# Kernel tuning notes

Hardware: AMD Instinct MI355X
Metric: run time of the kernel (lower is better)

Reference implementation:

```python
import jax, jax.numpy as jnp
import numpy as np

B, L, S, H, E = 4, 2048, 2048, 8, 64


def setup_inputs() -> dict:
    key = jax.random.key(0)
    kq, kk, kv, kt = jax.random.split(key, 4)
    queries = jax.random.normal(kq, (B, L, H, E), dtype=jnp.float32)
    keys = jax.random.normal(kk, (B, S, H, E), dtype=jnp.float32)
    values = jax.random.normal(kv, (B, S, H, E), dtype=jnp.float32)
    # de-stationarization log-scale factor, kept small so exp(tau) ~ O(1)
    tau = 0.1 * jax.random.normal(kt, (B, 1, 1, 1), dtype=jnp.float32)
    # causal mask: True above the diagonal (positions to be masked)
    attn_mask = jnp.triu(jnp.ones((L, S), dtype=bool), k=1)
    return {"queries": queries, "keys": keys, "values": values,
            "attn_mask": attn_mask, "tau": tau}


def reference(queries, keys, values, attn_mask, tau):
    # queries: [B,L,H,E], keys/values: [B,S,H,E], tau: [B,1,1,1], mask: [L,S]
    E_ = queries.shape[-1]
    scale = 1.0 / jnp.sqrt(jnp.asarray(E_, dtype=queries.dtype))
    # scores: [B,H,L,S], with tau-based de-stationarization rescale
    scores = jnp.einsum('blhe,bshe->bhls', queries, keys) * (scale * jnp.exp(tau))
    scores = jnp.where(attn_mask, -jnp.inf, scores)
    A = jax.nn.softmax(scores, axis=-1)  # dropout is identity at inference
    V = jnp.einsum('bhls,bshd->blhd', A, values)
    return V
```

## Files before the change

### kernel.cpp

```cpp
#include <hip/hip_runtime.h>
#include <hip/hip_bf16.h>
#include <math.h>

#define B_ 4
#define L_ 2048
#define H_ 8
#define E_ 64
#define HE 512

typedef short bf16x8 __attribute__((ext_vector_type(8)));
typedef float f32x4 __attribute__((ext_vector_type(4)));
typedef float f32x16 __attribute__((ext_vector_type(16)));
typedef unsigned short u16x4 __attribute__((ext_vector_type(4)));
typedef unsigned short u16x8 __attribute__((ext_vector_type(8)));

__device__ __forceinline__ unsigned short f2b(float f) {
  return __builtin_bit_cast(unsigned short, (__hip_bfloat16)f);
}
__device__ __forceinline__ unsigned cvtpk(float lo, float hi) {
  unsigned r;
  asm("v_cvt_pk_bf16_f32 %0, %1, %2" : "=v"(r) : "v"(lo), "v"(hi));
  return r;
}
__device__ __forceinline__ void pl32swap(unsigned &a, unsigned &b) {
  asm volatile("v_permlane32_swap_b32 %0, %1" : "+v"(a), "+v"(b));
}

__global__ __launch_bounds__(256, 2) void attn_fwd(
    const float* __restrict__ Q, const float* __restrict__ K,
    const float* __restrict__ V, const float* __restrict__ tau,
    float* __restrict__ O)
{
  const int f  = blockIdx.x + 16 * (blockIdx.y + 8 * blockIdx.z);
  const int u  = f >> 5, hb = f & 31;
  const int h  = hb & 7, b = hb >> 3;
  const int qt = (u < 8) ? u : 23 - u;

  const int tid  = threadIdx.x;
  const int wave = tid >> 6, lane = tid & 63;
  const int l31 = lane & 31, hi = lane >> 5;
  const int l7 = l31 & 7;

  __shared__ unsigned short ldsK[2][64 * 64];
  __shared__ unsigned short ldsV[2][64 * 64];

  const float qscale = 0.125f * expf(tau[b]) * 1.44269504088896f;
  const int q0w = qt * 128 + wave * 32;
  const int myq = q0w + l31;

  const float* Qb = Q + (((size_t)b * L_ + myq) * H_ + h) * E_;
  bf16x8 qf[4];
  #pragma unroll
  for (int ks = 0; ks < 4; ++ks) {
    f32x4 a = *(const f32x4*)(Qb + ks * 16 + hi * 8);
    f32x4 c = *(const f32x4*)(Qb + ks * 16 + hi * 8 + 4);
    #pragma unroll
    for (int j = 0; j < 4; ++j) {
      qf[ks][j]     = (short)f2b(a[j] * qscale);
      qf[ks][4 + j] = (short)f2b(c[j] * qscale);
    }
  }

  float m_run = -INFINITY, l_run = 0.0f;
  f32x16 oacc[2];
  #pragma unroll
  for (int nd = 0; nd < 2; ++nd)
    #pragma unroll
    for (int r = 0; r < 16; ++r) oacc[nd][r] = 0.0f;

  const int krow = tid >> 2, kcg = tid & 3;
  const int vkv = (tid & 15) * 4, vd = (tid >> 4) * 4;
  const float* Kp = K + ((size_t)b * L_ * H_ + h) * E_ + (size_t)krow * HE + kcg * 16;
  const float* Vp = V + ((size_t)b * L_ * H_ + h) * E_ + (size_t)vkv * HE + vd;
  const int kwo0 = krow * 64 + (((2 * kcg) ^ (krow & 7)) << 3);
  const int kwo1 = krow * 64 + (((2 * kcg + 1) ^ (krow & 7)) << 3);

  const int nt = 2 * qt + 2;
  const int tmaxw = 2 * qt + (wave >> 1);

  {
    f32x4 kq[4], vq[4];
    #pragma unroll
    for (int i = 0; i < 4; ++i) kq[i] = *(const f32x4*)(Kp + 4 * i);
    #pragma unroll
    for (int i = 0; i < 4; ++i) vq[i] = *(const f32x4*)(Vp + (size_t)i * HE);
    u16x8 w0, w1;
    #pragma unroll
    for (int j = 0; j < 4; ++j) {
      w0[j] = f2b(kq[0][j]); w0[4 + j] = f2b(kq[1][j]);
      w1[j] = f2b(kq[2][j]); w1[4 + j] = f2b(kq[3][j]);
    }
    *(u16x8*)(&ldsK[0][kwo0]) = w0;
    *(u16x8*)(&ldsK[0][kwo1]) = w1;
    #pragma unroll
    for (int jd = 0; jd < 4; ++jd) {
      const int row = vd + jd;
      u16x4 vw;
      #pragma unroll
      for (int i = 0; i < 4; ++i) vw[i] = f2b(vq[i][jd]);
      *(u16x4*)(&ldsV[0][row * 64 + (((vkv >> 3) ^ (row & 7)) << 3) + (vkv & 7)]) = vw;
    }
  }
  __syncthreads();
  int cur = 0;

  for (int t = 0; t < nt; ++t) {
    const bool havenext = (t + 1 < nt);
    f32x4 kq[4], vq[4];
    if (havenext) {
      const float* Kn = Kp + (size_t)(t + 1) * 64 * HE;
      const float* Vn = Vp + (size_t)(t + 1) * 64 * HE;
      #pragma unroll
      for (int i = 0; i < 4; ++i) kq[i] = *(const f32x4*)(Kn + 4 * i);
      #pragma unroll
      for (int i = 0; i < 4; ++i) vq[i] = *(const f32x4*)(Vn + (size_t)i * HE);
    }

    if (t <= tmaxw) {
      const unsigned short* Kl = ldsK[cur];
      const unsigned short* Vl = ldsV[cur];

      f32x16 sacc[2];
      #pragma unroll
      for (int mt = 0; mt < 2; ++mt)
        #pragma unroll
        for (int r = 0; r < 16; ++r) sacc[mt][r] = 0.0f;
      __builtin_amdgcn_s_setprio(1);
      #pragma unroll
      for (int ks = 0; ks < 4; ++ks) {
        #pragma unroll
        for (int mt = 0; mt < 2; ++mt) {
          bf16x8 kf = *(const bf16x8*)(Kl + (32 * mt + l31) * 64 +
                                       (((2 * ks + hi) ^ l7) << 3));
          sacc[mt] = __builtin_amdgcn_mfma_f32_32x32x16_bf16(kf, qf[ks], sacc[mt], 0, 0, 0);
        }
      }
      __builtin_amdgcn_s_setprio(0);

      if (t == tmaxw) {
        const int dq = myq - 64 * t;
        const int kvhi = 4 * hi;
        #pragma unroll
        for (int mt = 0; mt < 2; ++mt)
          #pragma unroll
          for (int r = 0; r < 16; ++r) {
            const int kvl = (r & 3) + 8 * (r >> 2) + 32 * mt;
            if (kvl + kvhi > dq) sacc[mt][r] = -3.0e38f;
          }
      }

      float p0 = sacc[0][0], p1 = sacc[0][1], p2 = sacc[0][2], p3 = sacc[0][3];
      #pragma unroll
      for (int mt = 0; mt < 2; ++mt)
        #pragma unroll
        for (int r = (mt == 0 ? 4 : 0); r < 16; r += 4) {
          p0 = fmaxf(p0, sacc[mt][r]);
          p1 = fmaxf(p1, sacc[mt][r + 1]);
          p2 = fmaxf(p2, sacc[mt][r + 2]);
          p3 = fmaxf(p3, sacc[mt][r + 3]);
        }
      float mx = fmaxf(fmaxf(p0, p1), fmaxf(p2, p3));
      mx = fmaxf(mx, __shfl_xor(mx, 32));

      if (!__all(mx - m_run <= 8.0f)) {
        const float mnew = fmaxf(m_run, mx);
        const float corr = exp2f(m_run - mnew);
        m_run = mnew;
        l_run *= corr;
        #pragma unroll
        for (int r = 0; r < 16; ++r) {
          const int qrow = (r & 3) + 8 * (r >> 2) + 4 * hi;
          const float cr = __shfl(corr, qrow);
          oacc[0][r] *= cr;
          oacc[1][r] *= cr;
        }
      }

      float s0 = 0.f, s1 = 0.f, s2 = 0.f, s3 = 0.f;
      #pragma unroll
      for (int mt = 0; mt < 2; ++mt)
        #pragma unroll
        for (int r = 0; r < 16; r += 4) {
          float e0 = exp2f(sacc[mt][r]     - m_run);
          float e1 = exp2f(sacc[mt][r + 1] - m_run);
          float e2 = exp2f(sacc[mt][r + 2] - m_run);
          float e3 = exp2f(sacc[mt][r + 3] - m_run);
          sacc[mt][r] = e0; sacc[mt][r + 1] = e1;
          sacc[mt][r + 2] = e2; sacc[mt][r + 3] = e3;
          s0 += e0; s1 += e1; s2 += e2; s3 += e3;
        }
      float rs = (s0 + s1) + (s2 + s3);
      rs += __shfl_xor(rs, 32);
      l_run += rs;

      unsigned pk0[8], pk1[8];
      #pragma unroll
      for (int i = 0; i < 8; ++i) pk0[i] = cvtpk(sacc[0][2 * i], sacc[0][2 * i + 1]);
      #pragma unroll
      for (int i = 0; i < 8; ++i) pk1[i] = cvtpk(sacc[1][2 * i], sacc[1][2 * i + 1]);
      bf16x8 pf[4];
      #pragma unroll
      for (int ks = 0; ks < 4; ++ks) {
        unsigned a  = (ks >> 1) ? pk1[4 * (ks & 1)]     : pk0[4 * (ks & 1)];
        unsigned y  = (ks >> 1) ? pk1[4 * (ks & 1) + 2] : pk0[4 * (ks & 1) + 2];
        unsigned a2 = (ks >> 1) ? pk1[4 * (ks & 1) + 1] : pk0[4 * (ks & 1) + 1];
        unsigned y2 = (ks >> 1) ? pk1[4 * (ks & 1) + 3] : pk0[4 * (ks & 1) + 3];
        pl32swap(a, y);
        pl32swap(a2, y2);
        union { unsigned w[4]; bf16x8 v; } pu;
        pu.w[0] = a; pu.w[1] = a2; pu.w[2] = y; pu.w[3] = y2;
        pf[ks] = pu.v;
      }

      __builtin_amdgcn_s_setprio(1);
      #pragma unroll
      for (int ks = 0; ks < 4; ++ks) {
        #pragma unroll
        for (int nd = 0; nd < 2; ++nd) {
          bf16x8 vf = *(const bf16x8*)(Vl + (32 * nd + l31) * 64 +
                                       (((2 * ks + hi) ^ l7) << 3));
          oacc[nd] = __builtin_amdgcn_mfma_f32_32x32x16_bf16(pf[ks], vf, oacc[nd], 0, 0, 0);
        }
      }
      __builtin_amdgcn_s_setprio(0);
    }

    if (havenext) {
      const int nb = cur ^ 1;
      u16x8 w0, w1;
      #pragma unroll
      for (int j = 0; j < 4; ++j) {
        w0[j] = f2b(kq[0][j]); w0[4 + j] = f2b(kq[1][j]);
        w1[j] = f2b(kq[2][j]); w1[4 + j] = f2b(kq[3][j]);
      }
      *(u16x8*)(&ldsK[nb][kwo0]) = w0;
      *(u16x8*)(&ldsK[nb][kwo1]) = w1;
      #pragma unroll
      for (int jd = 0; jd < 4; ++jd) {
        const int row = vd + jd;
        u16x4 vw;
        #pragma unroll
        for (int i = 0; i < 4; ++i) vw[i] = f2b(vq[i][jd]);
        *(u16x4*)(&ldsV[nb][row * 64 + (((vkv >> 3) ^ (row & 7)) << 3) + (vkv & 7)]) = vw;
      }
      __syncthreads();
      cur = nb;
    }
  }

  const float linv = 1.0f / l_run;
  float* Ob = O + (((size_t)b * L_ + q0w) * H_ + h) * E_;
  #pragma unroll
  for (int r = 0; r < 16; ++r) {
    const int qrow = (r & 3) + 8 * (r >> 2) + 4 * hi;
    const float inv = __shfl(linv, qrow);
    Ob[(size_t)qrow * HE + l31]      = oacc[0][r] * inv;
    Ob[(size_t)qrow * HE + 32 + l31] = oacc[1][r] * inv;
  }
}

extern "C" void kernel_launch(void* const* d_in, const int* in_sizes, int n_in,
                              void* d_out, int out_size, void* d_ws, size_t ws_size,
                              hipStream_t stream) {
  (void)in_sizes; (void)n_in; (void)out_size; (void)d_ws; (void)ws_size;
  const float* Q   = (const float*)d_in[0];
  const float* K   = (const float*)d_in[1];
  const float* V   = (const float*)d_in[2];
  const float* tau = (const float*)d_in[4];
  float* O = (float*)d_out;
  dim3 grid(L_ / 128, H_, B_), block(256);
  hipLaunchKernelGGL(attn_fwd, grid, block, 0, stream, Q, K, V, tau, O);
}
```

Measured before the change: 60.08 us.

## Widen KV tile to 128 keys per iteration with 16-way V swizzle

Each loop iteration now stages 128 keys and values into LDS instead of 64, which halves the number of iterations and barriers. The QK product now covers four 32-row tiles, and the PV product is reorganised over eight k-steps with a 128-wide transposed V layout and a 16-row XOR swizzle. Per-wave causal skipping is removed, so every wave computes the full final tile and relies on masking. This roughly doubles LDS use and register pressure (more score accumulators and prefetch registers), which may hurt occupancy at two blocks per CU.

```diff
diff --git a/kernel.cpp b/kernel.cpp
--- a/kernel.cpp
+++ b/kernel.cpp
@@ -41,12 +41,13 @@
   const int l31 = lane & 31, hi = lane >> 5;
   const int l7 = l31 & 7;
 
-  __shared__ unsigned short ldsK[2][64 * 64];
-  __shared__ unsigned short ldsV[2][64 * 64];
+  __shared__ unsigned short ldsK[2][128 * 64];
+  __shared__ unsigned short ldsV[2][64 * 128];
 
   const float qscale = 0.125f * expf(tau[b]) * 1.44269504088896f;
   const int q0w = qt * 128 + wave * 32;
   const int myq = q0w + l31;
+  const int dqd = 32 * wave + l31;
 
   const float* Qb = Q + (((size_t)b * L_ + myq) * H_ + h) * E_;
   bf16x8 qf[4];
@@ -72,33 +73,35 @@
   const int vkv = (tid & 15) * 4, vd = (tid >> 4) * 4;
   const float* Kp = K + ((size_t)b * L_ * H_ + h) * E_ + (size_t)krow * HE + kcg * 16;
   const float* Vp = V + ((size_t)b * L_ * H_ + h) * E_ + (size_t)vkv * HE + vd;
-  const int kwo0 = krow * 64 + (((2 * kcg) ^ (krow & 7)) << 3);
-  const int kwo1 = krow * 64 + (((2 * kcg + 1) ^ (krow & 7)) << 3);
-
-  const int nt = 2 * qt + 2;
-  const int tmaxw = 2 * qt + (wave >> 1);
-
-  {
-    f32x4 kq[4], vq[4];
-    #pragma unroll
-    for (int i = 0; i < 4; ++i) kq[i] = *(const f32x4*)(Kp + 4 * i);
-    #pragma unroll
-    for (int i = 0; i < 4; ++i) vq[i] = *(const f32x4*)(Vp + (size_t)i * HE);
+
+  const int nt = qt + 1;
+
+  f32x4 kq[2][4], vq[2][4];
+  #pragma unroll
+  for (int hf = 0; hf < 2; ++hf) {
+    #pragma unroll
+    for (int i = 0; i < 4; ++i) kq[hf][i] = *(const f32x4*)(Kp + hf * 64 * HE + 4 * i);
+    #pragma unroll
+    for (int i = 0; i < 4; ++i) vq[hf][i] = *(const f32x4*)(Vp + hf * 64 * HE + (size_t)i * HE);
+  }
+  #pragma unroll
+  for (int hf = 0; hf < 2; ++hf) {
+    const int r = krow + 64 * hf;
     u16x8 w0, w1;
     #pragma unroll
     for (int j = 0; j < 4; ++j) {
-      w0[j] = f2b(kq[0][j]); w0[4 + j] = f2b(kq[1][j]);
-      w1[j] = f2b(kq[2][j]); w1[4 + j] = f2b(kq[3][j]);
-    }
-    *(u16x8*)(&ldsK[0][kwo0]) = w0;
-    *(u16x8*)(&ldsK[0][kwo1]) = w1;
+      w0[j] = f2b(kq[hf][0][j]); w0[4 + j] = f2b(kq[hf][1][j]);
+      w1[j] = f2b(kq[hf][2][j]); w1[4 + j] = f2b(kq[hf][3][j]);
+    }
+    *(u16x8*)(&ldsK[0][r * 64 + (((2 * kcg) ^ (krow & 7)) << 3)]) = w0;
+    *(u16x8*)(&ldsK[0][r * 64 + (((2 * kcg + 1) ^ (krow & 7)) << 3)]) = w1;
     #pragma unroll
     for (int jd = 0; jd < 4; ++jd) {
       const int row = vd + jd;
       u16x4 vw;
       #pragma unroll
-      for (int i = 0; i < 4; ++i) vw[i] = f2b(vq[i][jd]);
-      *(u16x4*)(&ldsV[0][row * 64 + (((vkv >> 3) ^ (row & 7)) << 3) + (vkv & 7)]) = vw;
+      for (int i = 0; i < 4; ++i) vw[i] = f2b(vq[hf][i][jd]);
+      *(u16x4*)(&ldsV[0][row * 128 + ((((vkv >> 3) + 8 * hf) ^ (row & 15)) << 3) + (vkv & 7)]) = vw;
     }
   }
   __syncthreads();
@@ -106,142 +109,142 @@
 
   for (int t = 0; t < nt; ++t) {
     const bool havenext = (t + 1 < nt);
-    f32x4 kq[4], vq[4];
     if (havenext) {
-      const float* Kn = Kp + (size_t)(t + 1) * 64 * HE;
-      const float* Vn = Vp + (size_t)(t + 1) * 64 * HE;
-      #pragma unroll
-      for (int i = 0; i < 4; ++i) kq[i] = *(const f32x4*)(Kn + 4 * i);
-      #pragma unroll
-      for (int i = 0; i < 4; ++i) vq[i] = *(const f32x4*)(Vn + (size_t)i * HE);
-    }
-
-    if (t <= tmaxw) {
-      const unsigned short* Kl = ldsK[cur];
-      const unsigned short* Vl = ldsV[cur];
-
-      f32x16 sacc[2];
-      #pragma unroll
-      for (int mt = 0; mt < 2; ++mt)
-        #pragma unroll
-        for (int r = 0; r < 16; ++r) sacc[mt][r] = 0.0f;
-      __builtin_amdgcn_s_setprio(1);
-      #pragma unroll
-      for (int ks = 0; ks < 4; ++ks) {
-        #pragma unroll
-        for (int mt = 0; mt < 2; ++mt) {
-          bf16x8 kf = *(const bf16x8*)(Kl + (32 * mt + l31) * 64 +
-                                       (((2 * ks + hi) ^ l7) << 3));
-          sacc[mt] = __builtin_amdgcn_mfma_f32_32x32x16_bf16(kf, qf[ks], sacc[mt], 0, 0, 0);
+      const float* Kn = Kp + (size_t)(t + 1) * 128 * HE;
+      const float* Vn = Vp + (size_t)(t + 1) * 128 * HE;
+      #pragma unroll
+      for (int hf = 0; hf < 2; ++hf) {
+        #pragma unroll
+        for (int i = 0; i < 4; ++i) kq[hf][i] = *(const f32x4*)(Kn + hf * 64 * HE + 4 * i);
+        #pragma unroll
+        for (int i = 0; i < 4; ++i) vq[hf][i] = *(const f32x4*)(Vn + hf * 64 * HE + (size_t)i * HE);
+      }
+    }
+
+    const unsigned short* Kl = ldsK[cur];
+    const unsigned short* Vl = ldsV[cur];
+
+    f32x16 sacc[4];
+    #pragma unroll
+    for (int mt = 0; mt < 4; ++mt)
+      #pragma unroll
+      for (int r = 0; r < 16; ++r) sacc[mt][r] = 0.0f;
+    __builtin_amdgcn_s_setprio(1);
+    #pragma unroll
+    for (int ks = 0; ks < 4; ++ks) {
+      #pragma unroll
+      for (int mt = 0; mt < 4; ++mt) {
+        bf16x8 kf = *(const bf16x8*)(Kl + (32 * mt + l31) * 64 +
+                                     (((2 * ks + hi) ^ l7) << 3));
+        sacc[mt] = __builtin_amdgcn_mfma_f32_32x32x16_bf16(kf, qf[ks], sacc[mt], 0, 0, 0);
+      }
+    }
+    __builtin_amdgcn_s_setprio(0);
+
+    if (t == nt - 1) {
+      #pragma unroll
+      for (int mt = 0; mt < 4; ++mt)
+        #pragma unroll
+        for (int r = 0; r < 16; ++r) {
+          const int kvl = 32 * mt + (r & 3) + 8 * (r >> 2) + 4 * hi;
+          if (kvl > dqd) sacc[mt][r] = -3.0e38f;
         }
-      }
-      __builtin_amdgcn_s_setprio(0);
-
-      if (t == tmaxw) {
-        const int dq = myq - 64 * t;
-        const int kvhi = 4 * hi;
-        #pragma unroll
-        for (int mt = 0; mt < 2; ++mt)
-          #pragma unroll
-          for (int r = 0; r < 16; ++r) {
-            const int kvl = (r & 3) + 8 * (r >> 2) + 32 * mt;
-            if (kvl + kvhi > dq) sacc[mt][r] = -3.0e38f;
-          }
-      }
-
-      float p0 = sacc[0][0], p1 = sacc[0][1], p2 = sacc[0][2], p3 = sacc[0][3];
-      #pragma unroll
-      for (int mt = 0; mt < 2; ++mt)
-        #pragma unroll
-        for (int r = (mt == 0 ? 4 : 0); r < 16; r += 4) {
-          p0 = fmaxf(p0, sacc[mt][r]);
-          p1 = fmaxf(p1, sacc[mt][r + 1]);
-          p2 = fmaxf(p2, sacc[mt][r + 2]);
-          p3 = fmaxf(p3, sacc[mt][r + 3]);
-        }
-      float mx = fmaxf(fmaxf(p0, p1), fmaxf(p2, p3));
-      mx = fmaxf(mx, __shfl_xor(mx, 32));
-
-      if (!__all(mx - m_run <= 8.0f)) {
-        const float mnew = fmaxf(m_run, mx);
-        const float corr = exp2f(m_run - mnew);
-        m_run = mnew;
-        l_run *= corr;
-        #pragma unroll
-        for (int r = 0; r < 16; ++r) {
-          const int qrow = (r & 3) + 8 * (r >> 2) + 4 * hi;
-          const float cr = __shfl(corr, qrow);
-          oacc[0][r] *= cr;
-          oacc[1][r] *= cr;
-        }
-      }
-
-      float s0 = 0.f, s1 = 0.f, s2 = 0.f, s3 = 0.f;
-      #pragma unroll
-      for (int mt = 0; mt < 2; ++mt)
-        #pragma unroll
-        for (int r = 0; r < 16; r += 4) {
-          float e0 = exp2f(sacc[mt][r]     - m_run);
-          float e1 = exp2f(sacc[mt][r + 1] - m_run);
-          float e2 = exp2f(sacc[mt][r + 2] - m_run);
-          float e3 = exp2f(sacc[mt][r + 3] - m_run);
-          sacc[mt][r] = e0; sacc[mt][r + 1] = e1;
-          sacc[mt][r + 2] = e2; sacc[mt][r + 3] = e3;
-          s0 += e0; s1 += e1; s2 += e2; s3 += e3;
-        }
-      float rs = (s0 + s1) + (s2 + s3);
-      rs += __shfl_xor(rs, 32);
-      l_run += rs;
-
-      unsigned pk0[8], pk1[8];
-      #pragma unroll
-      for (int i = 0; i < 8; ++i) pk0[i] = cvtpk(sacc[0][2 * i], sacc[0][2 * i + 1]);
-      #pragma unroll
-      for (int i = 0; i < 8; ++i) pk1[i] = cvtpk(sacc[1][2 * i], sacc[1][2 * i + 1]);
-      bf16x8 pf[4];
-      #pragma unroll
-      for (int ks = 0; ks < 4; ++ks) {
-        unsigned a  = (ks >> 1) ? pk1[4 * (ks & 1)]     : pk0[4 * (ks & 1)];
-        unsigned y  = (ks >> 1) ? pk1[4 * (ks & 1) + 2] : pk0[4 * (ks & 1) + 2];
-        unsigned a2 = (ks >> 1) ? pk1[4 * (ks & 1) + 1] : pk0[4 * (ks & 1) + 1];
-        unsigned y2 = (ks >> 1) ? pk1[4 * (ks & 1) + 3] : pk0[4 * (ks & 1) + 3];
-        pl32swap(a, y);
-        pl32swap(a2, y2);
-        union { unsigned w[4]; bf16x8 v; } pu;
-        pu.w[0] = a; pu.w[1] = a2; pu.w[2] = y; pu.w[3] = y2;
-        pf[ks] = pu.v;
-      }
-
-      __builtin_amdgcn_s_setprio(1);
-      #pragma unroll
-      for (int ks = 0; ks < 4; ++ks) {
-        #pragma unroll
-        for (int nd = 0; nd < 2; ++nd) {
-          bf16x8 vf = *(const bf16x8*)(Vl + (32 * nd + l31) * 64 +
-                                       (((2 * ks + hi) ^ l7) << 3));
-          oacc[nd] = __builtin_amdgcn_mfma_f32_32x32x16_bf16(pf[ks], vf, oacc[nd], 0, 0, 0);
-        }
-      }
-      __builtin_amdgcn_s_setprio(0);
-    }
+    }
+
+    float p0 = sacc[0][0], p1 = sacc[0][1], p2 = sacc[0][2], p3 = sacc[0][3];
+    #pragma unroll
+    for (int mt = 0; mt < 4; ++mt)
+      #pragma unroll
+      for (int r = (mt == 0 ? 4 : 0); r < 16; r += 4) {
+        p0 = fmaxf(p0, sacc[mt][r]);
+        p1 = fmaxf(p1, sacc[mt][r + 1]);
+        p2 = fmaxf(p2, sacc[mt][r + 2]);
+        p3 = fmaxf(p3, sacc[mt][r + 3]);
+      }
+    float mx = fmaxf(fmaxf(p0, p1), fmaxf(p2, p3));
+    mx = fmaxf(mx, __shfl_xor(mx, 32));
+
+    if (!__all(mx - m_run <= 8.0f)) {
+      const float mnew = fmaxf(m_run, mx);
+      const float corr = exp2f(m_run - mnew);
+      m_run = mnew;
+      l_run *= corr;
+      #pragma unroll
+      for (int r = 0; r < 16; ++r) {
+        const int qrow = (r & 3) + 8 * (r >> 2) + 4 * hi;
+        const float cr = __shfl(corr, qrow);
+        oacc[0][r] *= cr;
+        oacc[1][r] *= cr;
+      }
+    }
+
+    float s0 = 0.f, s1 = 0.f, s2 = 0.f, s3 = 0.f;
+    #pragma unroll
+    for (int mt = 0; mt < 4; ++mt)
+      #pragma unroll
+      for (int r = 0; r < 16; r += 4) {
+        float e0 = exp2f(sacc[mt][r]     - m_run);
+        float e1 = exp2f(sacc[mt][r + 1] - m_run);
+        float e2 = exp2f(sacc[mt][r + 2] - m_run);
+        float e3 = exp2f(sacc[mt][r + 3] - m_run);
+        sacc[mt][r] = e0; sacc[mt][r + 1] = e1;
+        sacc[mt][r + 2] = e2; sacc[mt][r + 3] = e3;
+        s0 += e0; s1 += e1; s2 += e2; s3 += e3;
+      }
+    float rs = (s0 + s1) + (s2 + s3);
+    rs += __shfl_xor(rs, 32);
+    l_run += rs;
+
+    unsigned pk[4][8];
+    #pragma unroll
+    for (int mt = 0; mt < 4; ++mt)
+      #pragma unroll
+      for (int i = 0; i < 8; ++i)
+        pk[mt][i] = cvtpk(sacc[mt][2 * i], sacc[mt][2 * i + 1]);
+
+    __builtin_amdgcn_s_setprio(1);
+    #pragma unroll
+    for (int ks = 0; ks < 8; ++ks) {
+      const int c = ks & 1;
+      unsigned a  = pk[ks >> 1][4 * c];
+      unsigned y  = pk[ks >> 1][4 * c + 2];
+      unsigned a2 = pk[ks >> 1][4 * c + 1];
+      unsigned y2 = pk[ks >> 1][4 * c + 3];
+      pl32swap(a, y);
+      pl32swap(a2, y2);
+      union { unsigned w[4]; bf16x8 v; } pu;
+      pu.w[0] = a; pu.w[1] = a2; pu.w[2] = y; pu.w[3] = y2;
+      #pragma unroll
+      for (int nd = 0; nd < 2; ++nd) {
+        const int d = 32 * nd + l31;
+        bf16x8 vf = *(const bf16x8*)(Vl + d * 128 +
+                                     (((2 * ks + hi) ^ (d & 15)) << 3));
+        oacc[nd] = __builtin_amdgcn_mfma_f32_32x32x16_bf16(pu.v, vf, oacc[nd], 0, 0, 0);
+      }
+    }
+    __builtin_amdgcn_s_setprio(0);
 
     if (havenext) {
       const int nb = cur ^ 1;
-      u16x8 w0, w1;
-      #pragma unroll
-      for (int j = 0; j < 4; ++j) {
-        w0[j] = f2b(kq[0][j]); w0[4 + j] = f2b(kq[1][j]);
-        w1[j] = f2b(kq[2][j]); w1[4 + j] = f2b(kq[3][j]);
-      }
-      *(u16x8*)(&ldsK[nb][kwo0]) = w0;
-      *(u16x8*)(&ldsK[nb][kwo1]) = w1;
-      #pragma unroll
-      for (int jd = 0; jd < 4; ++jd) {
-        const int row = vd + jd;
-        u16x4 vw;
-        #pragma unroll
-        for (int i = 0; i < 4; ++i) vw[i] = f2b(vq[i][jd]);
-        *(u16x4*)(&ldsV[nb][row * 64 + (((vkv >> 3) ^ (row & 7)) << 3) + (vkv & 7)]) = vw;
+      #pragma unroll
+      for (int hf = 0; hf < 2; ++hf) {
+        const int r = krow + 64 * hf;
+        u16x8 w0, w1;
+        #pragma unroll
+        for (int j = 0; j < 4; ++j) {
+          w0[j] = f2b(kq[hf][0][j]); w0[4 + j] = f2b(kq[hf][1][j]);
+          w1[j] = f2b(kq[hf][2][j]); w1[4 + j] = f2b(kq[hf][3][j]);
+        }
+        *(u16x8*)(&ldsK[nb][r * 64 + (((2 * kcg) ^ (krow & 7)) << 3)]) = w0;
+        *(u16x8*)(&ldsK[nb][r * 64 + (((2 * kcg + 1) ^ (krow & 7)) << 3)]) = w1;
+        #pragma unroll
+        for (int jd = 0; jd < 4; ++jd) {
+          const int row = vd + jd;
+          u16x4 vw;
+          #pragma unroll
+          for (int i = 0; i < 4; ++i) vw[i] = f2b(vq[hf][i][jd]);
+          *(u16x4*)(&ldsV[nb][row * 128 + ((((vkv >> 3) + 8 * hf) ^ (row & 15)) << 3) + (vkv & 7)]) = vw;
+        }
       }
       __syncthreads();
       cur = nb;
```

Measured after the change: 63.86 us. +6.3%, slower.

## Split KV sequence across two wave groups per block and merge partial softmax

Applied to the files above, without the earlier changes.

Doubles the block to 512 threads so that two halves of 4 waves each process alternating 64-key tiles of the same 128-query tile. Each step now loads 128 keys, which halves the number of loop iterations and barriers per block. At the end the second half's partial outputs and row max/sum go to shared memory (a union with the KV buffers) and are merged flash-decoding style. The aim is more parallelism and latency hiding per query tile, at the cost of doubled LDS, an extra combine pass, and possible occupancy pressure from launch_bounds(512,4).

```diff
diff --git a/kernel.cpp b/kernel.cpp
--- a/kernel.cpp
+++ b/kernel.cpp
@@ -26,7 +26,7 @@
   asm volatile("v_permlane32_swap_b32 %0, %1" : "+v"(a), "+v"(b));
 }
 
-__global__ __launch_bounds__(256, 2) void attn_fwd(
+__global__ __launch_bounds__(512, 4) void attn_fwd(
     const float* __restrict__ Q, const float* __restrict__ K,
     const float* __restrict__ V, const float* __restrict__ tau,
     float* __restrict__ O)
@@ -40,13 +40,19 @@
   const int wave = tid >> 6, lane = tid & 63;
   const int l31 = lane & 31, hi = lane >> 5;
   const int l7 = l31 & 7;
-
-  __shared__ unsigned short ldsK[2][64 * 64];
-  __shared__ unsigned short ldsV[2][64 * 64];
+  const int half = wave >> 2, wv = wave & 3;
+
+  __shared__ union {
+    struct { unsigned short Kt[2][2][64 * 64];
+             unsigned short Vt[2][2][64 * 64]; } kv;
+    struct { float O[128][64]; float m[128]; float l[128]; } cmb;
+  } sm;
 
   const float qscale = 0.125f * expf(tau[b]) * 1.44269504088896f;
-  const int q0w = qt * 128 + wave * 32;
+  const int q0w = qt * 128 + wv * 32;
   const int myq = q0w + l31;
+  const int dqd = 32 * wv + l31 - 64 * half;
+  const bool skipw = (half == 1) && (wv < 2);
 
   const float* Qb = Q + (((size_t)b * L_ + myq) * H_ + h) * E_;
   bf16x8 qf[4];
@@ -68,37 +74,38 @@
     #pragma unroll
     for (int r = 0; r < 16; ++r) oacc[nd][r] = 0.0f;
 
-  const int krow = tid >> 2, kcg = tid & 3;
-  const int vkv = (tid & 15) * 4, vd = (tid >> 4) * 4;
-  const float* Kp = K + ((size_t)b * L_ * H_ + h) * E_ + (size_t)krow * HE + kcg * 16;
-  const float* Vp = V + ((size_t)b * L_ * H_ + h) * E_ + (size_t)vkv * HE + vd;
-  const int kwo0 = krow * 64 + (((2 * kcg) ^ (krow & 7)) << 3);
+  const int hs = tid >> 8, st = tid & 255;
+  const int krow = st >> 2, kcg = st & 3;
+  const int vkv = (st & 15) * 4, vd = (st >> 4) * 4;
+  const size_t bh = ((size_t)b * L_ * H_ + h) * E_;
+  const float* Kp = K + bh + (size_t)(64 * hs + krow) * HE + kcg * 16;
+  const float* Vp = V + bh + (size_t)(64 * hs + vkv) * HE + vd;
+  const int kwo0 = krow * 64 + (((2 * kcg)     ^ (krow & 7)) << 3);
   const int kwo1 = krow * 64 + (((2 * kcg + 1) ^ (krow & 7)) << 3);
 
-  const int nt = 2 * qt + 2;
-  const int tmaxw = 2 * qt + (wave >> 1);
-
+  const int nt = qt + 1;
+
+  f32x4 kq[4], vq[4];
+  #pragma unroll
+  for (int i = 0; i < 4; ++i) kq[i] = *(const f32x4*)(Kp + 4 * i);
+  #pragma unroll
+  for (int i = 0; i < 4; ++i) vq[i] = *(const f32x4*)(Vp + (size_t)i * HE);
   {
-    f32x4 kq[4], vq[4];
-    #pragma unroll
-    for (int i = 0; i < 4; ++i) kq[i] = *(const f32x4*)(Kp + 4 * i);
-    #pragma unroll
-    for (int i = 0; i < 4; ++i) vq[i] = *(const f32x4*)(Vp + (size_t)i * HE);
     u16x8 w0, w1;
     #pragma unroll
     for (int j = 0; j < 4; ++j) {
       w0[j] = f2b(kq[0][j]); w0[4 + j] = f2b(kq[1][j]);
       w1[j] = f2b(kq[2][j]); w1[4 + j] = f2b(kq[3][j]);
     }
-    *(u16x8*)(&ldsK[0][kwo0]) = w0;
-    *(u16x8*)(&ldsK[0][kwo1]) = w1;
+    *(u16x8*)(&sm.kv.Kt[hs][0][kwo0]) = w0;
+    *(u16x8*)(&sm.kv.Kt[hs][0][kwo1]) = w1;
     #pragma unroll
     for (int jd = 0; jd < 4; ++jd) {
       const int row = vd + jd;
       u16x4 vw;
       #pragma unroll
       for (int i = 0; i < 4; ++i) vw[i] = f2b(vq[i][jd]);
-      *(u16x4*)(&ldsV[0][row * 64 + (((vkv >> 3) ^ (row & 7)) << 3) + (vkv & 7)]) = vw;
+      *(u16x4*)(&sm.kv.Vt[hs][0][row * 64 + (((vkv >> 3) ^ (row & 7)) << 3) + (vkv & 7)]) = vw;
     }
   }
   __syncthreads();
@@ -106,19 +113,18 @@
 
   for (int t = 0; t < nt; ++t) {
     const bool havenext = (t + 1 < nt);
-    f32x4 kq[4], vq[4];
     if (havenext) {
-      const float* Kn = Kp + (size_t)(t + 1) * 64 * HE;
-      const float* Vn = Vp + (size_t)(t + 1) * 64 * HE;
+      const float* Kn = Kp + (size_t)(t + 1) * 128 * HE;
+      const float* Vn = Vp + (size_t)(t + 1) * 128 * HE;
       #pragma unroll
       for (int i = 0; i < 4; ++i) kq[i] = *(const f32x4*)(Kn + 4 * i);
       #pragma unroll
       for (int i = 0; i < 4; ++i) vq[i] = *(const f32x4*)(Vn + (size_t)i * HE);
     }
 
-    if (t <= tmaxw) {
-      const unsigned short* Kl = ldsK[cur];
-      const unsigned short* Vl = ldsV[cur];
+    if (!(skipw && t == nt - 1)) {
+      const unsigned short* Kl = sm.kv.Kt[half][cur];
+      const unsigned short* Vl = sm.kv.Vt[half][cur];
 
       f32x16 sacc[2];
       #pragma unroll
@@ -137,15 +143,13 @@
       }
       __builtin_amdgcn_s_setprio(0);
 
-      if (t == tmaxw) {
-        const int dq = myq - 64 * t;
-        const int kvhi = 4 * hi;
+      if (t == nt - 1) {
         #pragma unroll
         for (int mt = 0; mt < 2; ++mt)
           #pragma unroll
           for (int r = 0; r < 16; ++r) {
-            const int kvl = (r & 3) + 8 * (r >> 2) + 32 * mt;
-            if (kvl + kvhi > dq) sacc[mt][r] = -3.0e38f;
+            const int kvl = 32 * mt + (r & 3) + 8 * (r >> 2) + 4 * hi;
+            if (kvl > dqd) sacc[mt][r] = -3.0e38f;
           }
       }
 
@@ -193,33 +197,30 @@
       rs += __shfl_xor(rs, 32);
       l_run += rs;
 
-      unsigned pk0[8], pk1[8];
-      #pragma unroll
-      for (int i = 0; i < 8; ++i) pk0[i] = cvtpk(sacc[0][2 * i], sacc[0][2 * i + 1]);
-      #pragma unroll
-      for (int i = 0; i < 8; ++i) pk1[i] = cvtpk(sacc[1][2 * i], sacc[1][2 * i + 1]);
-      bf16x8 pf[4];
+      unsigned pk[2][8];
+      #pragma unroll
+      for (int mt = 0; mt < 2; ++mt)
+        #pragma unroll
+        for (int i = 0; i < 8; ++i)
+          pk[mt][i] = cvtpk(sacc[mt][2 * i], sacc[mt][2 * i + 1]);
+
+      __builtin_amdgcn_s_setprio(1);
       #pragma unroll
       for (int ks = 0; ks < 4; ++ks) {
-        unsigned a  = (ks >> 1) ? pk1[4 * (ks & 1)]     : pk0[4 * (ks & 1)];
-        unsigned y  = (ks >> 1) ? pk1[4 * (ks & 1) + 2] : pk0[4 * (ks & 1) + 2];
-        unsigned a2 = (ks >> 1) ? pk1[4 * (ks & 1) + 1] : pk0[4 * (ks & 1) + 1];
-        unsigned y2 = (ks >> 1) ? pk1[4 * (ks & 1) + 3] : pk0[4 * (ks & 1) + 3];
+        const int c = ks & 1, mtx = ks >> 1;
+        unsigned a  = pk[mtx][4 * c];
+        unsigned y  = pk[mtx][4 * c + 2];
+        unsigned a2 = pk[mtx][4 * c + 1];
+        unsigned y2 = pk[mtx][4 * c + 3];
         pl32swap(a, y);
         pl32swap(a2, y2);
         union { unsigned w[4]; bf16x8 v; } pu;
         pu.w[0] = a; pu.w[1] = a2; pu.w[2] = y; pu.w[3] = y2;
-        pf[ks] = pu.v;
-      }
-
-      __builtin_amdgcn_s_setprio(1);
-      #pragma unroll
-      for (int ks = 0; ks < 4; ++ks) {
         #pragma unroll
         for (int nd = 0; nd < 2; ++nd) {
           bf16x8 vf = *(const bf16x8*)(Vl + (32 * nd + l31) * 64 +
                                        (((2 * ks + hi) ^ l7) << 3));
-          oacc[nd] = __builtin_amdgcn_mfma_f32_32x32x16_bf16(pf[ks], vf, oacc[nd], 0, 0, 0);
+          oacc[nd] = __builtin_amdgcn_mfma_f32_32x32x16_bf16(pu.v, vf, oacc[nd], 0, 0, 0);
         }
       }
       __builtin_amdgcn_s_setprio(0);
@@ -233,29 +234,51 @@
         w0[j] = f2b(kq[0][j]); w0[4 + j] = f2b(kq[1][j]);
         w1[j] = f2b(kq[2][j]); w1[4 + j] = f2b(kq[3][j]);
       }
-      *(u16x8*)(&ldsK[nb][kwo0]) = w0;
-      *(u16x8*)(&ldsK[nb][kwo1]) = w1;
+      *(u16x8*)(&sm.kv.Kt[hs][nb][kwo0]) = w0;
+      *(u16x8*)(&sm.kv.Kt[hs][nb][kwo1]) = w1;
       #pragma unroll
       for (int jd = 0; jd < 4; ++jd) {
         const int row = vd + jd;
         u16x4 vw;
         #pragma unroll
         for (int i = 0; i < 4; ++i) vw[i] = f2b(vq[i][jd]);
-        *(u16x4*)(&ldsV[nb][row * 64 + (((vkv >> 3) ^ (row & 7)) << 3) + (vkv & 7)]) = vw;
+        *(u16x4*)(&sm.kv.Vt[hs][nb][row * 64 + (((vkv >> 3) ^ (row & 7)) << 3) + (vkv & 7)]) = vw;
       }
       __syncthreads();
       cur = nb;
     }
   }
 
-  const float linv = 1.0f / l_run;
-  float* Ob = O + (((size_t)b * L_ + q0w) * H_ + h) * E_;
-  #pragma unroll
-  for (int r = 0; r < 16; ++r) {
-    const int qrow = (r & 3) + 8 * (r >> 2) + 4 * hi;
-    const float inv = __shfl(linv, qrow);
-    Ob[(size_t)qrow * HE + l31]      = oacc[0][r] * inv;
-    Ob[(size_t)qrow * HE + 32 + l31] = oacc[1][r] * inv;
+  __syncthreads();
+  if (half == 1) {
+    #pragma unroll
+    for (int r = 0; r < 16; ++r) {
+      const int qrow = (r & 3) + 8 * (r >> 2) + 4 * hi;
+      sm.cmb.O[32 * wv + qrow][l31]      = oacc[0][r];
+      sm.cmb.O[32 * wv + qrow][32 + l31] = oacc[1][r];
+    }
+    if (hi == 0) { sm.cmb.m[32 * wv + l31] = m_run; sm.cmb.l[32 * wv + l31] = l_run; }
+  }
+  __syncthreads();
+  if (half == 0) {
+    const float m_b = sm.cmb.m[32 * wv + l31];
+    const float l_b = sm.cmb.l[32 * wv + l31];
+    const float mm = fmaxf(m_run, m_b);
+    const float sa = exp2f(m_run - mm);
+    const float sb = exp2f(m_b - mm);
+    const float linv = 1.0f / (sa * l_run + sb * l_b);
+    const float wa = sa * linv, wb = sb * linv;
+    float* Ob = O + (((size_t)b * L_ + q0w) * H_ + h) * E_;
+    #pragma unroll
+    for (int r = 0; r < 16; ++r) {
+      const int qrow = (r & 3) + 8 * (r >> 2) + 4 * hi;
+      const float wa_r = __shfl(wa, qrow);
+      const float wb_r = __shfl(wb, qrow);
+      Ob[(size_t)qrow * HE + l31] =
+          wa_r * oacc[0][r] + wb_r * sm.cmb.O[32 * wv + qrow][l31];
+      Ob[(size_t)qrow * HE + 32 + l31] =
+          wa_r * oacc[1][r] + wb_r * sm.cmb.O[32 * wv + qrow][32 + l31];
+    }
   }
 }
 
@@ -268,6 +291,6 @@
   const float* V   = (const float*)d_in[2];
   const float* tau = (const float*)d_in[4];
   float* O = (float*)d_out;
-  dim3 grid(L_ / 128, H_, B_), block(256);
+  dim3 grid(L_ / 128, H_, B_), block(512);
   hipLaunchKernelGGL(attn_fwd, grid, block, 0, stream, Q, K, V, tau, O);
 }
```

After: 123.8 us. 106% more time.

## Software-pipeline QK of next tile with softmax/PV of current using triple LDS buffers

Applied to the files above, without the earlier changes.

Restructures the KV loop into a three-stage pipeline: the global load for tile t+2, the QK MFMA for tile t+1 and the softmax plus PV for tile t are issued in the same iteration. LDS buffers grow from two to three so tile t+1 can be read while tile t+2 is staged. The loop is unrolled by two with ping-ponged score registers. The aim is to overlap the softmax exp work with matrix-core work, at the cost of more LDS and VGPR pressure, which may reduce occupancy or cause spills.

```diff
diff --git a/kernel.cpp b/kernel.cpp
--- a/kernel.cpp
+++ b/kernel.cpp
@@ -41,8 +41,8 @@
   const int l31 = lane & 31, hi = lane >> 5;
   const int l7 = l31 & 7;
 
-  __shared__ unsigned short ldsK[2][64 * 64];
-  __shared__ unsigned short ldsV[2][64 * 64];
+  __shared__ unsigned short ldsK[3][64 * 64];
+  __shared__ unsigned short ldsV[3][64 * 64];
 
   const float qscale = 0.125f * expf(tau[b]) * 1.44269504088896f;
   const int q0w = qt * 128 + wave * 32;
@@ -70,182 +70,165 @@
 
   const int krow = tid >> 2, kcg = tid & 3;
   const int vkv = (tid & 15) * 4, vd = (tid >> 4) * 4;
-  const float* Kp = K + ((size_t)b * L_ * H_ + h) * E_ + (size_t)krow * HE + kcg * 16;
-  const float* Vp = V + ((size_t)b * L_ * H_ + h) * E_ + (size_t)vkv * HE + vd;
-  const int kwo0 = krow * 64 + (((2 * kcg) ^ (krow & 7)) << 3);
+  const size_t bh = ((size_t)b * L_ * H_ + h) * E_;
+  const float* Kp = K + bh + (size_t)krow * HE + kcg * 16;
+  const float* Vp = V + bh + (size_t)vkv * HE + vd;
+  const int kwo0 = krow * 64 + (((2 * kcg)     ^ (krow & 7)) << 3);
   const int kwo1 = krow * 64 + (((2 * kcg + 1) ^ (krow & 7)) << 3);
 
   const int nt = 2 * qt + 2;
   const int tmaxw = 2 * qt + (wave >> 1);
 
-  {
-    f32x4 kq[4], vq[4];
-    #pragma unroll
-    for (int i = 0; i < 4; ++i) kq[i] = *(const f32x4*)(Kp + 4 * i);
-    #pragma unroll
-    for (int i = 0; i < 4; ++i) vq[i] = *(const f32x4*)(Vp + (size_t)i * HE);
+  auto load_tile = [&](int t, f32x4 (&kq)[4], f32x4 (&vq)[4]) {
+    const float* Kn = Kp + (size_t)t * 64 * HE;
+    const float* Vn = Vp + (size_t)t * 64 * HE;
+    #pragma unroll
+    for (int i = 0; i < 4; ++i) kq[i] = *(const f32x4*)(Kn + 4 * i);
+    #pragma unroll
+    for (int i = 0; i < 4; ++i) vq[i] = *(const f32x4*)(Vn + (size_t)i * HE);
+  };
+  auto stage_write = [&](int nb, const f32x4 (&kq)[4], const f32x4 (&vq)[4]) {
     u16x8 w0, w1;
     #pragma unroll
     for (int j = 0; j < 4; ++j) {
       w0[j] = f2b(kq[0][j]); w0[4 + j] = f2b(kq[1][j]);
       w1[j] = f2b(kq[2][j]); w1[4 + j] = f2b(kq[3][j]);
     }
-    *(u16x8*)(&ldsK[0][kwo0]) = w0;
-    *(u16x8*)(&ldsK[0][kwo1]) = w1;
+    *(u16x8*)(&ldsK[nb][kwo0]) = w0;
+    *(u16x8*)(&ldsK[nb][kwo1]) = w1;
     #pragma unroll
     for (int jd = 0; jd < 4; ++jd) {
       const int row = vd + jd;
       u16x4 vw;
       #pragma unroll
       for (int i = 0; i < 4; ++i) vw[i] = f2b(vq[i][jd]);
-      *(u16x4*)(&ldsV[0][row * 64 + (((vkv >> 3) ^ (row & 7)) << 3) + (vkv & 7)]) = vw;
-    }
-  }
-  __syncthreads();
-  int cur = 0;
-
-  for (int t = 0; t < nt; ++t) {
-    const bool havenext = (t + 1 < nt);
-    f32x4 kq[4], vq[4];
-    if (havenext) {
-      const float* Kn = Kp + (size_t)(t + 1) * 64 * HE;
-      const float* Vn = Vp + (size_t)(t + 1) * 64 * HE;
-      #pragma unroll
-      for (int i = 0; i < 4; ++i) kq[i] = *(const f32x4*)(Kn + 4 * i);
-      #pragma unroll
-      for (int i = 0; i < 4; ++i) vq[i] = *(const f32x4*)(Vn + (size_t)i * HE);
-    }
-
-    if (t <= tmaxw) {
-      const unsigned short* Kl = ldsK[cur];
-      const unsigned short* Vl = ldsV[cur];
-
-      f32x16 sacc[2];
+      *(u16x4*)(&ldsV[nb][row * 64 + (((vkv >> 3) ^ (row & 7)) << 3) + (vkv & 7)]) = vw;
+    }
+  };
+  auto qk = [&](int bn, f32x16 (&s)[2]) {
+    const unsigned short* Kl = ldsK[bn];
+    #pragma unroll
+    for (int mt = 0; mt < 2; ++mt)
+      #pragma unroll
+      for (int r = 0; r < 16; ++r) s[mt][r] = 0.0f;
+    __builtin_amdgcn_s_setprio(1);
+    #pragma unroll
+    for (int ks = 0; ks < 4; ++ks) {
+      #pragma unroll
+      for (int mt = 0; mt < 2; ++mt) {
+        bf16x8 kf = *(const bf16x8*)(Kl + (32 * mt + l31) * 64 +
+                                     (((2 * ks + hi) ^ l7) << 3));
+        s[mt] = __builtin_amdgcn_mfma_f32_32x32x16_bf16(kf, qf[ks], s[mt], 0, 0, 0);
+      }
+    }
+    __builtin_amdgcn_s_setprio(0);
+  };
+  auto soft_pv = [&](int t, int bc, f32x16 (&s)[2]) {
+    if (t == tmaxw) {
+      const int dq = myq - 64 * t;
       #pragma unroll
       for (int mt = 0; mt < 2; ++mt)
         #pragma unroll
-        for (int r = 0; r < 16; ++r) sacc[mt][r] = 0.0f;
-      __builtin_amdgcn_s_setprio(1);
-      #pragma unroll
-      for (int ks = 0; ks < 4; ++ks) {
-        #pragma unroll
-        for (int mt = 0; mt < 2; ++mt) {
-          bf16x8 kf = *(const bf16x8*)(Kl + (32 * mt + l31) * 64 +
-                                       (((2 * ks + hi) ^ l7) << 3));
-          sacc[mt] = __builtin_amdgcn_mfma_f32_32x32x16_bf16(kf, qf[ks], sacc[mt], 0, 0, 0);
+        for (int r = 0; r < 16; ++r) {
+          const int kvl = 32 * mt + (r & 3) + 8 * (r >> 2) + 4 * hi;
+          if (kvl > dq) s[mt][r] = -3.0e38f;
         }
-      }
-      __builtin_amdgcn_s_setprio(0);
-
-      if (t == tmaxw) {
-        const int dq = myq - 64 * t;
-        const int kvhi = 4 * hi;
-        #pragma unroll
-        for (int mt = 0; mt < 2; ++mt)
-          #pragma unroll
-          for (int r = 0; r < 16; ++r) {
-            const int kvl = (r & 3) + 8 * (r >> 2) + 32 * mt;
-            if (kvl + kvhi > dq) sacc[mt][r] = -3.0e38f;
-          }
-      }
-
-      float p0 = sacc[0][0], p1 = sacc[0][1], p2 = sacc[0][2], p3 = sacc[0][3];
-      #pragma unroll
-      for (int mt = 0; mt < 2; ++mt)
-        #pragma unroll
-        for (int r = (mt == 0 ? 4 : 0); r < 16; r += 4) {
-          p0 = fmaxf(p0, sacc[mt][r]);
-          p1 = fmaxf(p1, sacc[mt][r + 1]);
-          p2 = fmaxf(p2, sacc[mt][r + 2]);
-          p3 = fmaxf(p3, sacc[mt][r + 3]);
-        }
-      float mx = fmaxf(fmaxf(p0, p1), fmaxf(p2, p3));
-      mx = fmaxf(mx, __shfl_xor(mx, 32));
-
-      if (!__all(mx - m_run <= 8.0f)) {
-        const float mnew = fmaxf(m_run, mx);
-        const float corr = exp2f(m_run - mnew);
-        m_run = mnew;
-        l_run *= corr;
-        #pragma unroll
-        for (int r = 0; r < 16; ++r) {
-          const int qrow = (r & 3) + 8 * (r >> 2) + 4 * hi;
-          const float cr = __shfl(corr, qrow);
-          oacc[0][r] *= cr;
-          oacc[1][r] *= cr;
-        }
-      }
-
-      float s0 = 0.f, s1 = 0.f, s2 = 0.f, s3 = 0.f;
-      #pragma unroll
-      for (int mt = 0; mt < 2; ++mt)
-        #pragma unroll
-        for (int r = 0; r < 16; r += 4) {
-          float e0 = exp2f(sacc[mt][r]     - m_run);
-          float e1 = exp2f(sacc[mt][r + 1] - m_run);
-          float e2 = exp2f(sacc[mt][r + 2] - m_run);
-          float e3 = exp2f(sacc[mt][r + 3] - m_run);
-          sacc[mt][r] = e0; sacc[mt][r + 1] = e1;
-          sacc[mt][r + 2] = e2; sacc[mt][r + 3] = e3;
-          s0 += e0; s1 += e1; s2 += e2; s3 += e3;
-        }
-      float rs = (s0 + s1) + (s2 + s3);
-      rs += __shfl_xor(rs, 32);
-      l_run += rs;
-
-      unsigned pk0[8], pk1[8];
-      #pragma unroll
-      for (int i = 0; i < 8; ++i) pk0[i] = cvtpk(sacc[0][2 * i], sacc[0][2 * i + 1]);
-      #pragma unroll
-      for (int i = 0; i < 8; ++i) pk1[i] = cvtpk(sacc[1][2 * i], sacc[1][2 * i + 1]);
-      bf16x8 pf[4];
-      #pragma unroll
-      for (int ks = 0; ks < 4; ++ks) {
-        unsigned a  = (ks >> 1) ? pk1[4 * (ks & 1)]     : pk0[4 * (ks & 1)];
-        unsigned y  = (ks >> 1) ? pk1[4 * (ks & 1) + 2] : pk0[4 * (ks & 1) + 2];
-        unsigned a2 = (ks >> 1) ? pk1[4 * (ks & 1) + 1] : pk0[4 * (ks & 1) + 1];
-        unsigned y2 = (ks >> 1) ? pk1[4 * (ks & 1) + 3] : pk0[4 * (ks & 1) + 3];
-        pl32swap(a, y);
-        pl32swap(a2, y2);
-        union { unsigned w[4]; bf16x8 v; } pu;
-        pu.w[0] = a; pu.w[1] = a2; pu.w[2] = y; pu.w[3] = y2;
-        pf[ks] = pu.v;
-      }
-
-      __builtin_amdgcn_s_setprio(1);
-      #pragma unroll
-      for (int ks = 0; ks < 4; ++ks) {
-        #pragma unroll
-        for (int nd = 0; nd < 2; ++nd) {
-          bf16x8 vf = *(const bf16x8*)(Vl + (32 * nd + l31) * 64 +
-                                       (((2 * ks + hi) ^ l7) << 3));
-          oacc[nd] = __builtin_amdgcn_mfma_f32_32x32x16_bf16(pf[ks], vf, oacc[nd], 0, 0, 0);
-        }
-      }
-      __builtin_amdgcn_s_setprio(0);
-    }
-
-    if (havenext) {
-      const int nb = cur ^ 1;
-      u16x8 w0, w1;
-      #pragma unroll
-      for (int j = 0; j < 4; ++j) {
-        w0[j] = f2b(kq[0][j]); w0[4 + j] = f2b(kq[1][j]);
-        w1[j] = f2b(kq[2][j]); w1[4 + j] = f2b(kq[3][j]);
-      }
-      *(u16x8*)(&ldsK[nb][kwo0]) = w0;
-      *(u16x8*)(&ldsK[nb][kwo1]) = w1;
-      #pragma unroll
-      for (int jd = 0; jd < 4; ++jd) {
-        const int row = vd + jd;
-        u16x4 vw;
-        #pragma unroll
-        for (int i = 0; i < 4; ++i) vw[i] = f2b(vq[i][jd]);
-        *(u16x4*)(&ldsV[nb][row * 64 + (((vkv >> 3) ^ (row & 7)) << 3) + (vkv & 7)]) = vw;
-      }
-      __syncthreads();
-      cur = nb;
-    }
+    }
+    float p0 = s[0][0], p1 = s[0][1], p2 = s[0][2], p3 = s[0][3];
+    #pragma unroll
+    for (int mt = 0; mt < 2; ++mt)
+      #pragma unroll
+      for (int r = (mt == 0 ? 4 : 0); r < 16; r += 4) {
+        p0 = fmaxf(p0, s[mt][r]);
+        p1 = fmaxf(p1, s[mt][r + 1]);
+        p2 = fmaxf(p2, s[mt][r + 2]);
+        p3 = fmaxf(p3, s[mt][r + 3]);
+      }
+    float mx = fmaxf(fmaxf(p0, p1), fmaxf(p2, p3));
+    mx = fmaxf(mx, __shfl_xor(mx, 32));
+    if (!__all(mx - m_run <= 8.0f)) {
+      const float mnew = fmaxf(m_run, mx);
+      const float corr = exp2f(m_run - mnew);
+      m_run = mnew;
+      l_run *= corr;
+      #pragma unroll
+      for (int r = 0; r < 16; ++r) {
+        const int qrow = (r & 3) + 8 * (r >> 2) + 4 * hi;
+        const float cr = __shfl(corr, qrow);
+        oacc[0][r] *= cr;
+        oacc[1][r] *= cr;
+      }
+    }
+    float s0 = 0.f, s1 = 0.f, s2 = 0.f, s3 = 0.f;
+    #pragma unroll
+    for (int mt = 0; mt < 2; ++mt)
+      #pragma unroll
+      for (int r = 0; r < 16; r += 4) {
+        float e0 = exp2f(s[mt][r]     - m_run);
+        float e1 = exp2f(s[mt][r + 1] - m_run);
+        float e2 = exp2f(s[mt][r + 2] - m_run);
+        float e3 = exp2f(s[mt][r + 3] - m_run);
+        s[mt][r] = e0; s[mt][r + 1] = e1;
+        s[mt][r + 2] = e2; s[mt][r + 3] = e3;
+        s0 += e0; s1 += e1; s2 += e2; s3 += e3;
+      }
+    float rs = (s0 + s1) + (s2 + s3);
+    rs += __shfl_xor(rs, 32);
+    l_run += rs;
+    unsigned pk[2][8];
+    #pragma unroll
+    for (int mt = 0; mt < 2; ++mt)
+      #pragma unroll
+      for (int i = 0; i < 8; ++i)
+        pk[mt][i] = cvtpk(s[mt][2 * i], s[mt][2 * i + 1]);
+    const unsigned short* Vl = ldsV[bc];
+    __builtin_amdgcn_s_setprio(1);
+    #pragma unroll
+    for (int ks = 0; ks < 4; ++ks) {
+      const int c = ks & 1, mtx = ks >> 1;
+      unsigned a  = pk[mtx][4 * c];
+      unsigned y  = pk[mtx][4 * c + 2];
+      unsigned a2 = pk[mtx][4 * c + 1];
+      unsigned y2 = pk[mtx][4 * c + 3];
+      pl32swap(a, y);
+      pl32swap(a2, y2);
+      union { unsigned w[4]; bf16x8 v; } pu;
+      pu.w[0] = a; pu.w[1] = a2; pu.w[2] = y; pu.w[3] = y2;
+      #pragma unroll
+      for (int nd = 0; nd < 2; ++nd) {
+        bf16x8 vf = *(const bf16x8*)(Vl + (32 * nd + l31) * 64 +
+                                     (((2 * ks + hi) ^ l7) << 3));
+        oacc[nd] = __builtin_amdgcn_mfma_f32_32x32x16_bf16(pu.v, vf, oacc[nd], 0, 0, 0);
+      }
+    }
+    __builtin_amdgcn_s_setprio(0);
+  };
+
+  f32x16 sA[2], sB[2];
+  {
+    f32x4 k0[4], v0[4], k1[4], v1[4];
+    load_tile(0, k0, v0);
+    load_tile(1, k1, v1);
+    stage_write(0, k0, v0);
+    __syncthreads();
+    qk(0, sA);
+    stage_write(1, k1, v1);
+    __syncthreads();
+  }
+
+  auto body = [&](int t, f32x16 (&scur)[2], f32x16 (&snxt)[2]) {
+    const int bc = t % 3, bn = (t + 1) % 3, bs = (t + 2) % 3;
+    f32x4 kq[4], vq[4];
+    const bool stage = (t + 2 < nt);
+    if (stage) load_tile(t + 2, kq, vq);
+    if ((t + 1 < nt) && (t + 1 <= tmaxw)) qk(bn, snxt);
+    if (t <= tmaxw) soft_pv(t, bc, scur);
+    if (stage) stage_write(bs, kq, vq);
+    __syncthreads();
+  };
+  for (int t = 0; t < nt; t += 2) {
+    body(t, sA, sB);
+    body(t + 1, sB, sA);
   }
 
   const float linv = 1.0f / l_run;
```

New measurement: 61.33 us. 2.1% more time.
